# Optimization experiments

Measured on AMD Instinct MI355X. Metric: run time of the kernel, lower is better.

The kernel has to match this reference:

```python
import math
import jax, jax.numpy as jnp
import numpy as np

K = 4          # beats_per_bar
POS_DIM = 32   # fourier pos-embed dim


def setup_inputs() -> dict:
    key = jax.random.key(0)
    k1, k2, k3 = jax.random.split(key, 3)
    B, M, D = 8, 8192, 1024
    beat_emb = jax.random.normal(k1, (B, M, D), dtype=jnp.float32)
    W = jax.random.normal(k2, (D, D + POS_DIM), dtype=jnp.float32) * 0.02  # nn.Linear weight [out, in]
    b = jax.random.normal(k3, (D,), dtype=jnp.float32) * 0.02
    return {"beat_emb": beat_emb, "W": W, "b": b}


def _fourier_features(pos, dim):
    # pos: [Mb] in [0,1] -> [Mb, dim] (dim even, so no zero-pad branch needed)
    half = dim // 2
    freqs = jnp.exp(jnp.linspace(0.0, math.log(1000.0), half)).astype(pos.dtype)
    ang = pos[:, None] * freqs  # [Mb, half]
    return jnp.concatenate([jnp.sin(ang), jnp.cos(ang)], axis=-1)


def reference(beat_emb, W, b):
    B, M, D = beat_emb.shape
    Mb = (M + K - 1) // K
    pad = Mb * K - M
    x = jnp.pad(beat_emb, ((0, 0), (0, pad), (0, 0))) if pad else beat_emb
    # fused segment mean: [B, Mb, K, D] -> sum -> divide by actual segment length
    sums = x.reshape(B, Mb, K, D).sum(axis=2)
    counts = jnp.minimum(K, M - jnp.arange(Mb) * K).astype(beat_emb.dtype)  # [Mb]
    out = sums / counts[None, :, None]  # [B, Mb, D]
    # fourier positional features on normalized bar index (same for every batch row)
    idx = jnp.arange(Mb, dtype=beat_emb.dtype)
    pos = jnp.clip(idx / max(1, Mb - 1), 0.0, 1.0)
    ff = _fourier_features(pos, POS_DIM)                     # [Mb, POS_DIM]
    ff = jnp.broadcast_to(ff[None], (B, Mb, POS_DIM))
    h = jnp.concatenate([out, ff], axis=-1)                  # [B, Mb, D+POS_DIM]
    return jnp.einsum('bmi,oi->bmo', h, W) + b               # Linear: x @ W.T + b
```

## Files before the change

kernel.cpp:

```cpp
#include <hip/hip_runtime.h>
#include <math.h>
#include <stdint.h>
#include <stddef.h>

typedef short bf16x8 __attribute__((ext_vector_type(8)));
typedef short bf16x4 __attribute__((ext_vector_type(4)));
typedef float f32x4  __attribute__((ext_vector_type(4)));

#define BATCH   8
#define D_IN    1024
#define POSD    32
#define KD      1056
#define KP      1088
#define MBARS   2048
#define MROWS   16384
#define NOUT    1024

__device__ __forceinline__ short f2bf(float f) {
    unsigned u = __builtin_bit_cast(unsigned, f);
    u += 0x7fffu + ((u >> 16) & 1u);
    return (short)(u >> 16);
}

__device__ __forceinline__ void async_load16(const short* g, short* l) {
    __builtin_amdgcn_global_load_lds((__attribute__((address_space(1))) void*)g,
                                     (__attribute__((address_space(3))) void*)l,
                                     16, 0, 0);
}

__global__ __launch_bounds__(256) void prep(const float* __restrict__ x,
                                            const float* __restrict__ W,
                                            short* __restrict__ h,
                                            short* __restrict__ Wb) {
    const int t = threadIdx.x;
    const int bid = blockIdx.x;
    if (bid < MROWS) {
        const float4* src = (const float4*)(x + (size_t)bid * 4096);
        float4 s0 = src[t], s1 = src[t + 256], s2 = src[t + 512], s3 = src[t + 768];
        bf16x4 o = { f2bf((s0.x + s1.x + s2.x + s3.x) * 0.25f),
                     f2bf((s0.y + s1.y + s2.y + s3.y) * 0.25f),
                     f2bf((s0.z + s1.z + s2.z + s3.z) * 0.25f),
                     f2bf((s0.w + s1.w + s2.w + s3.w) * 0.25f) };
        short* hr = h + (size_t)bid * KP;
        *(bf16x4*)(hr + t * 4) = o;
        if (t < POSD) {
            const int mb = bid & (MBARS - 1);
            float pos = (float)mb * (1.0f / (float)(MBARS - 1));
            float fr  = expf((float)(t & 15) * (6.907755278982137f / 15.0f));
            float ang = pos * fr;
            hr[D_IN + t] = f2bf((t < 16) ? sinf(ang) : cosf(ang));
            hr[KD + t]   = 0;
        }
    } else {
        const int r = bid - MROWS;
        const float* wr = W + (size_t)r * KD;
        short* br = Wb + (size_t)r * KP;
        float4 v = *(const float4*)(wr + t * 4);
        bf16x4 o = { f2bf(v.x), f2bf(v.y), f2bf(v.z), f2bf(v.w) };
        *(bf16x4*)(br + t * 4) = o;
        if (t < 8) {
            float4 u = *(const float4*)(wr + 1024 + t * 4);
            bf16x4 p = { f2bf(u.x), f2bf(u.y), f2bf(u.z), f2bf(u.w) };
            *(bf16x4*)(br + 1024 + t * 4) = p;
            *(bf16x4*)(br + KD + t * 4)   = (bf16x4){0, 0, 0, 0};
        }
    }
}

__global__ __launch_bounds__(256) void gemm_bt(const short* __restrict__ A,
                                               const short* __restrict__ B,
                                               const float* __restrict__ bias,
                                               float* __restrict__ C) {
    __shared__ short As[128 * 64];
    __shared__ short Bs[128 * 64];

    const int tid  = threadIdx.x;
    const int wave = tid >> 6;
    const int lane = tid & 63;
    const int wrow = wave >> 1;
    const int wcol = wave & 1;

    const int m0 = blockIdx.x * 128;
    const int n0 = blockIdx.y * 128;

    const int r8   = tid >> 3;
    const int soct = (tid & 7) ^ (r8 & 7);
    const short* ag = A + (size_t)(m0 + r8) * KP + soct * 8;
    const short* bg = B + (size_t)(n0 + r8) * KP + soct * 8;
    short* al = As + wave * 512;
    short* bl = Bs + wave * 512;

    const int r  = lane & 15;
    const int q  = lane >> 4;
    const int rx = r & 7;
    const short* afr = As + (wrow * 64 + r) * 64;
    const short* bfr = Bs + (wcol * 64 + r) * 64;
    const int sl0 = ((q    ) ^ rx) * 8;
    const int sl1 = ((4 + q) ^ rx) * 8;

    f32x4 acc[4][4] = {};

    for (int k0 = 0; k0 < KP; k0 += 64) {
        __syncthreads();
#pragma unroll
        for (int i = 0; i < 4; ++i) {
            async_load16(ag + k0 + (size_t)i * 32 * KP, al + i * 2048);
            async_load16(bg + k0 + (size_t)i * 32 * KP, bl + i * 2048);
        }
        __syncthreads();

#pragma unroll
        for (int s = 0; s < 2; ++s) {
            const int sl = s ? sl1 : sl0;
            bf16x8 a[4], b[4];
#pragma unroll
            for (int i = 0; i < 4; ++i) {
                a[i] = *(const bf16x8*)(afr + i * 1024 + sl);
                b[i] = *(const bf16x8*)(bfr + i * 1024 + sl);
            }
#pragma unroll
            for (int i = 0; i < 4; ++i)
#pragma unroll
                for (int j = 0; j < 4; ++j)
                    acc[i][j] = __builtin_amdgcn_mfma_f32_16x16x32_bf16(a[i], b[j], acc[i][j], 0, 0, 0);
        }
    }

    const int rr0 = m0 + wrow * 64 + (q << 2);
    const int c0  = n0 + wcol * 64 + r;
    float bv[4];
#pragma unroll
    for (int j = 0; j < 4; ++j) bv[j] = bias[c0 + j * 16];
#pragma unroll
    for (int i = 0; i < 4; ++i)
#pragma unroll
        for (int rg = 0; rg < 4; ++rg) {
            float* cp = C + (size_t)(rr0 + i * 16 + rg) * NOUT;
#pragma unroll
            for (int j = 0; j < 4; ++j)
                cp[c0 + j * 16] = acc[i][j][rg] + bv[j];
        }
}

extern "C" void kernel_launch(void* const* d_in, const int* in_sizes, int n_in,
                              void* d_out, int out_size, void* d_ws, size_t ws_size,
                              hipStream_t stream) {
    const float* x    = (const float*)d_in[0];
    const float* W    = (const float*)d_in[1];
    const float* bias = (const float*)d_in[2];
    float* out = (float*)d_out;

    short* Wb = (short*)d_ws;
    short* h  = (short*)((char*)d_ws + (size_t)NOUT * KP * sizeof(short));

    prep   <<<dim3(MROWS + NOUT), dim3(256), 0, stream>>>(x, W, h, Wb);
    gemm_bt<<<dim3(MROWS / 128, NOUT / 128), dim3(256), 0, stream>>>(h, Wb, bias, out);
}
```

Measured before the change: 423.0 us.

## Fuse segment-mean into GEMM and precompute Fourier-feature projection table

The segment-mean reduction and bf16 conversion move into the GEMM's A-tile load, so the intermediate h matrix is no longer written to and re-read from global memory. The Fourier-feature columns are removed from the GEMM's K dimension. Their contribution is precomputed once per bar as a 2048x1024 fp32 table with the bias folded in, then added in the epilogue. The GEMM now uses 64-row by full-1024-column tiles with 512 threads, holding the whole W slice in LDS. In exchange, occupancy is low, W traffic per block is large, and the x loads are synchronous with no double buffering.

Result: slower. 466.3 us (+10.2%).

```diff
diff --git a/kernel.cpp b/kernel.cpp
--- a/kernel.cpp
+++ b/kernel.cpp
@@ -8,10 +8,9 @@
 typedef float f32x4  __attribute__((ext_vector_type(4)));
 
 #define BATCH   8
-#define D_IN    1024
+#define D       1024
 #define POSD    32
-#define KD      1056
-#define KP      1088
+#define WIN     1056
 #define MBARS   2048
 #define MROWS   16384
 #define NOUT    1024
@@ -28,117 +27,134 @@
                                      16, 0, 0);
 }
 
-__global__ __launch_bounds__(256) void prep(const float* __restrict__ x,
-                                            const float* __restrict__ W,
-                                            short* __restrict__ h,
-                                            short* __restrict__ Wb) {
-    const int t = threadIdx.x;
+__global__ __launch_bounds__(256) void prep2(const float* __restrict__ W,
+                                             const float* __restrict__ bias,
+                                             short* __restrict__ Wb,
+                                             float* __restrict__ FFW) {
+    const int t   = threadIdx.x;
     const int bid = blockIdx.x;
-    if (bid < MROWS) {
-        const float4* src = (const float4*)(x + (size_t)bid * 4096);
-        float4 s0 = src[t], s1 = src[t + 256], s2 = src[t + 512], s3 = src[t + 768];
-        bf16x4 o = { f2bf((s0.x + s1.x + s2.x + s3.x) * 0.25f),
-                     f2bf((s0.y + s1.y + s2.y + s3.y) * 0.25f),
-                     f2bf((s0.z + s1.z + s2.z + s3.z) * 0.25f),
-                     f2bf((s0.w + s1.w + s2.w + s3.w) * 0.25f) };
-        short* hr = h + (size_t)bid * KP;
-        *(bf16x4*)(hr + t * 4) = o;
-        if (t < POSD) {
-            const int mb = bid & (MBARS - 1);
-            float pos = (float)mb * (1.0f / (float)(MBARS - 1));
-            float fr  = expf((float)(t & 15) * (6.907755278982137f / 15.0f));
-            float ang = pos * fr;
-            hr[D_IN + t] = f2bf((t < 16) ? sinf(ang) : cosf(ang));
-            hr[KD + t]   = 0;
+    if (bid < NOUT) {
+        const float* wr = W + (size_t)bid * WIN;
+        float4 v = ((const float4*)wr)[t];
+        bf16x4 o = { f2bf(v.x), f2bf(v.y), f2bf(v.z), f2bf(v.w) };
+        *(bf16x4*)(Wb + (size_t)bid * D + t * 4) = o;
+    } else {
+        const int mb0 = (bid - NOUT) * 8;
+        __shared__ float ff[8][32];
+        if (t < 32) {
+            float fr = expf((float)(t & 15) * (6.907755278982137f / 15.0f));
+#pragma unroll
+            for (int e = 0; e < 8; ++e) {
+                float pos = (float)(mb0 + e) * (1.0f / (float)(MBARS - 1));
+                float ang = pos * fr;
+                ff[e][t] = (t < 16) ? sinf(ang) : cosf(ang);
+            }
         }
-    } else {
-        const int r = bid - MROWS;
-        const float* wr = W + (size_t)r * KD;
-        short* br = Wb + (size_t)r * KP;
-        float4 v = *(const float4*)(wr + t * 4);
-        bf16x4 o = { f2bf(v.x), f2bf(v.y), f2bf(v.z), f2bf(v.w) };
-        *(bf16x4*)(br + t * 4) = o;
-        if (t < 8) {
-            float4 u = *(const float4*)(wr + 1024 + t * 4);
-            bf16x4 p = { f2bf(u.x), f2bf(u.y), f2bf(u.z), f2bf(u.w) };
-            *(bf16x4*)(br + 1024 + t * 4) = p;
-            *(bf16x4*)(br + KD + t * 4)   = (bf16x4){0, 0, 0, 0};
+        __syncthreads();
+#pragma unroll
+        for (int u = 0; u < 4; ++u) {
+            const int n = t + u * 256;
+            const float* wp = W + (size_t)n * WIN + D;
+            float4 wv[8];
+#pragma unroll
+            for (int blk = 0; blk < 8; ++blk) wv[blk] = ((const float4*)wp)[blk];
+            const float bn = bias[n];
+#pragma unroll
+            for (int e = 0; e < 8; ++e) {
+                float s = bn;
+#pragma unroll
+                for (int blk = 0; blk < 8; ++blk) {
+                    s += ff[e][blk * 4 + 0] * wv[blk].x + ff[e][blk * 4 + 1] * wv[blk].y
+                       + ff[e][blk * 4 + 2] * wv[blk].z + ff[e][blk * 4 + 3] * wv[blk].w;
+                }
+                FFW[(size_t)(mb0 + e) * NOUT + n] = s;
+            }
         }
     }
 }
 
-__global__ __launch_bounds__(256) void gemm_bt(const short* __restrict__ A,
-                                               const short* __restrict__ B,
-                                               const float* __restrict__ bias,
-                                               float* __restrict__ C) {
-    __shared__ short As[128 * 64];
-    __shared__ short Bs[128 * 64];
+__global__ __launch_bounds__(512, 2) void fused(const float* __restrict__ x,
+                                                const short* __restrict__ Wb,
+                                                const float* __restrict__ FFW,
+                                                float* __restrict__ out) {
+    __shared__ short As[64 * 64];
+    __shared__ short Bs[1024 * 64];
 
     const int tid  = threadIdx.x;
     const int wave = tid >> 6;
     const int lane = tid & 63;
-    const int wrow = wave >> 1;
-    const int wcol = wave & 1;
+    const int m0   = blockIdx.x * 64;
 
-    const int m0 = blockIdx.x * 128;
-    const int n0 = blockIdx.y * 128;
-
-    const int r8   = tid >> 3;
-    const int soct = (tid & 7) ^ (r8 & 7);
-    const short* ag = A + (size_t)(m0 + r8) * KP + soct * 8;
-    const short* bg = B + (size_t)(n0 + r8) * KP + soct * 8;
-    short* al = As + wave * 512;
+    const int ra = tid >> 3;
+    const int oa = tid & 7;
+    const float* xg = x + (size_t)(m0 + ra) * 4096 + oa * 8;
+    short* aw = As + ra * 64 + ((oa ^ (ra & 7)) << 3);
+    const short* bg = Wb + (size_t)ra * D + ((oa ^ (ra & 7)) << 3);
     short* bl = Bs + wave * 512;
 
     const int r  = lane & 15;
     const int q  = lane >> 4;
     const int rx = r & 7;
-    const short* afr = As + (wrow * 64 + r) * 64;
-    const short* bfr = Bs + (wcol * 64 + r) * 64;
-    const int sl0 = ((q    ) ^ rx) * 8;
-    const int sl1 = ((4 + q) ^ rx) * 8;
+    const short* afr = As + r * 64;
+    const short* bfr = Bs + (wave * 128 + r) * 64;
+    const int sl0 = ((q    ) ^ rx) << 3;
+    const int sl1 = ((4 + q) ^ rx) << 3;
 
-    f32x4 acc[4][4] = {};
+    f32x4 acc[4][8] = {};
 
-    for (int k0 = 0; k0 < KP; k0 += 64) {
+    for (int k0 = 0; k0 < D; k0 += 64) {
         __syncthreads();
+        float4 t00 = *(const float4*)(xg + k0);
+        float4 t01 = *(const float4*)(xg + k0 + 4);
+        float4 t10 = *(const float4*)(xg + k0 + 1024);
+        float4 t11 = *(const float4*)(xg + k0 + 1028);
+        float4 t20 = *(const float4*)(xg + k0 + 2048);
+        float4 t21 = *(const float4*)(xg + k0 + 2052);
+        float4 t30 = *(const float4*)(xg + k0 + 3072);
+        float4 t31 = *(const float4*)(xg + k0 + 3076);
 #pragma unroll
-        for (int i = 0; i < 4; ++i) {
-            async_load16(ag + k0 + (size_t)i * 32 * KP, al + i * 2048);
-            async_load16(bg + k0 + (size_t)i * 32 * KP, bl + i * 2048);
-        }
+        for (int i = 0; i < 16; ++i)
+            async_load16(bg + k0 + (size_t)i * 64 * D, bl + i * 4096);
+        bf16x8 av = { f2bf((t00.x + t10.x + t20.x + t30.x) * 0.25f),
+                      f2bf((t00.y + t10.y + t20.y + t30.y) * 0.25f),
+                      f2bf((t00.z + t10.z + t20.z + t30.z) * 0.25f),
+                      f2bf((t00.w + t10.w + t20.w + t30.w) * 0.25f),
+                      f2bf((t01.x + t11.x + t21.x + t31.x) * 0.25f),
+                      f2bf((t01.y + t11.y + t21.y + t31.y) * 0.25f),
+                      f2bf((t01.z + t11.z + t21.z + t31.z) * 0.25f),
+                      f2bf((t01.w + t11.w + t21.w + t31.w) * 0.25f) };
+        *(bf16x8*)aw = av;
         __syncthreads();
 
 #pragma unroll
         for (int s = 0; s < 2; ++s) {
             const int sl = s ? sl1 : sl0;
-            bf16x8 a[4], b[4];
+            bf16x8 a[4], b[8];
 #pragma unroll
-            for (int i = 0; i < 4; ++i) {
-                a[i] = *(const bf16x8*)(afr + i * 1024 + sl);
-                b[i] = *(const bf16x8*)(bfr + i * 1024 + sl);
-            }
+            for (int i = 0; i < 4; ++i) a[i] = *(const bf16x8*)(afr + i * 1024 + sl);
+#pragma unroll
+            for (int j = 0; j < 8; ++j) b[j] = *(const bf16x8*)(bfr + j * 1024 + sl);
 #pragma unroll
             for (int i = 0; i < 4; ++i)
 #pragma unroll
-                for (int j = 0; j < 4; ++j)
+                for (int j = 0; j < 8; ++j)
                     acc[i][j] = __builtin_amdgcn_mfma_f32_16x16x32_bf16(a[i], b[j], acc[i][j], 0, 0, 0);
         }
     }
 
-    const int rr0 = m0 + wrow * 64 + (q << 2);
-    const int c0  = n0 + wcol * 64 + r;
-    float bv[4];
-#pragma unroll
-    for (int j = 0; j < 4; ++j) bv[j] = bias[c0 + j * 16];
+    const int mbb = m0 & (MBARS - 1);
+    const int c0  = wave * 128 + r;
+    const int rt0 = q << 2;
 #pragma unroll
     for (int i = 0; i < 4; ++i)
 #pragma unroll
         for (int rg = 0; rg < 4; ++rg) {
-            float* cp = C + (size_t)(rr0 + i * 16 + rg) * NOUT;
+            const int rt = i * 16 + rt0 + rg;
+            const float* fw = FFW + (size_t)(mbb + rt) * NOUT + c0;
+            float* cp = out + (size_t)(m0 + rt) * NOUT + c0;
 #pragma unroll
-            for (int j = 0; j < 4; ++j)
-                cp[c0 + j * 16] = acc[i][j][rg] + bv[j];
+            for (int j = 0; j < 8; ++j)
+                cp[j * 16] = acc[i][j][rg] + fw[j * 16];
         }
 }
 
@@ -150,9 +166,9 @@
     const float* bias = (const float*)d_in[2];
     float* out = (float*)d_out;
 
-    short* Wb = (short*)d_ws;
-    short* h  = (short*)((char*)d_ws + (size_t)NOUT * KP * sizeof(short));
+    short* Wb  = (short*)d_ws;
+    float* FFW = (float*)((char*)d_ws + (size_t)NOUT * D * sizeof(short));
 
-    prep   <<<dim3(MROWS + NOUT), dim3(256), 0, stream>>>(x, W, h, Wb);
-    gemm_bt<<<dim3(MROWS / 128, NOUT / 128), dim3(256), 0, stream>>>(h, Wb, bias, out);
+    prep2<<<dim3(NOUT + MBARS / 8), dim3(256), 0, stream>>>(W, bias, Wb, FFW);
+    fused<<<dim3(MROWS / 64), dim3(512), 0, stream>>>(x, Wb, FFW, out);
 }
```

## Precompute Fourier-feature projection plus bias per bar, shrink GEMM K to 1024

Applied to the files above, without the earlier changes.

Since the positional Fourier features are identical for every batch row, their product with the last 32 columns of W plus the bias is precomputed once per bar into an [MBARS, NOUT] float table. The main bf16 GEMM then runs over K=1024 instead of the padded 1088, which removes one of the 17 K-tiles. The epilogue adds the table entry for each row instead of the bias. The cost is an 8 MB fp32 table read in the epilogue and an extra small matmul in the prep kernel.

Measured after the change: 434.5 us. +2.7%, slower.

```diff
diff --git a/kernel.cpp b/kernel.cpp
--- a/kernel.cpp
+++ b/kernel.cpp
@@ -8,10 +8,9 @@
 typedef float f32x4  __attribute__((ext_vector_type(4)));
 
 #define BATCH   8
-#define D_IN    1024
+#define D       1024
 #define POSD    32
-#define KD      1056
-#define KP      1088
+#define WIN     1056
 #define MBARS   2048
 #define MROWS   16384
 #define NOUT    1024
@@ -28,11 +27,13 @@
                                      16, 0, 0);
 }
 
-__global__ __launch_bounds__(256) void prep(const float* __restrict__ x,
-                                            const float* __restrict__ W,
-                                            short* __restrict__ h,
-                                            short* __restrict__ Wb) {
-    const int t = threadIdx.x;
+__global__ __launch_bounds__(256) void prep3(const float* __restrict__ x,
+                                             const float* __restrict__ W,
+                                             const float* __restrict__ bias,
+                                             short* __restrict__ h,
+                                             short* __restrict__ Wb,
+                                             float* __restrict__ FFW) {
+    const int t   = threadIdx.x;
     const int bid = blockIdx.x;
     if (bid < MROWS) {
         const float4* src = (const float4*)(x + (size_t)bid * 4096);
@@ -41,35 +42,50 @@
                      f2bf((s0.y + s1.y + s2.y + s3.y) * 0.25f),
                      f2bf((s0.z + s1.z + s2.z + s3.z) * 0.25f),
                      f2bf((s0.w + s1.w + s2.w + s3.w) * 0.25f) };
-        short* hr = h + (size_t)bid * KP;
-        *(bf16x4*)(hr + t * 4) = o;
-        if (t < POSD) {
-            const int mb = bid & (MBARS - 1);
-            float pos = (float)mb * (1.0f / (float)(MBARS - 1));
-            float fr  = expf((float)(t & 15) * (6.907755278982137f / 15.0f));
-            float ang = pos * fr;
-            hr[D_IN + t] = f2bf((t < 16) ? sinf(ang) : cosf(ang));
-            hr[KD + t]   = 0;
+        *(bf16x4*)(h + (size_t)bid * D + t * 4) = o;
+    } else if (bid < MROWS + NOUT) {
+        const int rw = bid - MROWS;
+        float4 v = ((const float4*)(W + (size_t)rw * WIN))[t];
+        bf16x4 o = { f2bf(v.x), f2bf(v.y), f2bf(v.z), f2bf(v.w) };
+        *(bf16x4*)(Wb + (size_t)rw * D + t * 4) = o;
+    } else {
+        const int mb0 = (bid - MROWS - NOUT) * 8;
+        __shared__ float ff[8][32];
+        if (t < 32) {
+            float fr = expf((float)(t & 15) * (6.907755278982137f / 15.0f));
+#pragma unroll
+            for (int e = 0; e < 8; ++e) {
+                float pos = (float)(mb0 + e) * (1.0f / (float)(MBARS - 1));
+                float ang = pos * fr;
+                ff[e][t] = (t < 16) ? sinf(ang) : cosf(ang);
+            }
         }
-    } else {
-        const int r = bid - MROWS;
-        const float* wr = W + (size_t)r * KD;
-        short* br = Wb + (size_t)r * KP;
-        float4 v = *(const float4*)(wr + t * 4);
-        bf16x4 o = { f2bf(v.x), f2bf(v.y), f2bf(v.z), f2bf(v.w) };
-        *(bf16x4*)(br + t * 4) = o;
-        if (t < 8) {
-            float4 u = *(const float4*)(wr + 1024 + t * 4);
-            bf16x4 p = { f2bf(u.x), f2bf(u.y), f2bf(u.z), f2bf(u.w) };
-            *(bf16x4*)(br + 1024 + t * 4) = p;
-            *(bf16x4*)(br + KD + t * 4)   = (bf16x4){0, 0, 0, 0};
+        __syncthreads();
+#pragma unroll
+        for (int u = 0; u < 4; ++u) {
+            const int n = t + u * 256;
+            const float* wp = W + (size_t)n * WIN + D;
+            float4 wv[8];
+#pragma unroll
+            for (int blk = 0; blk < 8; ++blk) wv[blk] = ((const float4*)wp)[blk];
+            const float bn = bias[n];
+#pragma unroll
+            for (int e = 0; e < 8; ++e) {
+                float s = bn;
+#pragma unroll
+                for (int blk = 0; blk < 8; ++blk) {
+                    s += ff[e][blk * 4 + 0] * wv[blk].x + ff[e][blk * 4 + 1] * wv[blk].y
+                       + ff[e][blk * 4 + 2] * wv[blk].z + ff[e][blk * 4 + 3] * wv[blk].w;
+                }
+                FFW[(size_t)(mb0 + e) * NOUT + n] = s;
+            }
         }
     }
 }
 
 __global__ __launch_bounds__(256) void gemm_bt(const short* __restrict__ A,
                                                const short* __restrict__ B,
-                                               const float* __restrict__ bias,
+                                               const float* __restrict__ FFW,
                                                float* __restrict__ C) {
     __shared__ short As[128 * 64];
     __shared__ short Bs[128 * 64];
@@ -85,8 +101,8 @@
 
     const int r8   = tid >> 3;
     const int soct = (tid & 7) ^ (r8 & 7);
-    const short* ag = A + (size_t)(m0 + r8) * KP + soct * 8;
-    const short* bg = B + (size_t)(n0 + r8) * KP + soct * 8;
+    const short* ag = A + (size_t)(m0 + r8) * D + soct * 8;
+    const short* bg = B + (size_t)(n0 + r8) * D + soct * 8;
     short* al = As + wave * 512;
     short* bl = Bs + wave * 512;
 
@@ -100,12 +116,12 @@
 
     f32x4 acc[4][4] = {};
 
-    for (int k0 = 0; k0 < KP; k0 += 64) {
+    for (int k0 = 0; k0 < D; k0 += 64) {
         __syncthreads();
 #pragma unroll
         for (int i = 0; i < 4; ++i) {
-            async_load16(ag + k0 + (size_t)i * 32 * KP, al + i * 2048);
-            async_load16(bg + k0 + (size_t)i * 32 * KP, bl + i * 2048);
+            async_load16(ag + k0 + (size_t)i * 32 * D, al + i * 2048);
+            async_load16(bg + k0 + (size_t)i * 32 * D, bl + i * 2048);
         }
         __syncthreads();
 
@@ -128,17 +144,16 @@
 
     const int rr0 = m0 + wrow * 64 + (q << 2);
     const int c0  = n0 + wcol * 64 + r;
-    float bv[4];
-#pragma unroll
-    for (int j = 0; j < 4; ++j) bv[j] = bias[c0 + j * 16];
 #pragma unroll
     for (int i = 0; i < 4; ++i)
 #pragma unroll
         for (int rg = 0; rg < 4; ++rg) {
-            float* cp = C + (size_t)(rr0 + i * 16 + rg) * NOUT;
+            const int row = rr0 + i * 16 + rg;
+            const float* fw = FFW + (size_t)(row & (MBARS - 1)) * NOUT + c0;
+            float* cp = C + (size_t)row * NOUT + c0;
 #pragma unroll
             for (int j = 0; j < 4; ++j)
-                cp[c0 + j * 16] = acc[i][j][rg] + bv[j];
+                cp[j * 16] = acc[i][j][rg] + fw[j * 16];
         }
 }
 
@@ -150,9 +165,10 @@
     const float* bias = (const float*)d_in[2];
     float* out = (float*)d_out;
 
-    short* Wb = (short*)d_ws;
-    short* h  = (short*)((char*)d_ws + (size_t)NOUT * KP * sizeof(short));
+    short* Wb  = (short*)d_ws;
+    float* FFW = (float*)((char*)d_ws + (size_t)NOUT * D * sizeof(short));
+    short* h   = (short*)((char*)FFW + (size_t)MBARS * NOUT * sizeof(float));
 
-    prep   <<<dim3(MROWS + NOUT), dim3(256), 0, stream>>>(x, W, h, Wb);
-    gemm_bt<<<dim3(MROWS / 128, NOUT / 128), dim3(256), 0, stream>>>(h, Wb, bias, out);
+    prep3  <<<dim3(MROWS + NOUT + MBARS / 8), dim3(256), 0, stream>>>(x, W, bias, h, Wb, FFW);
+    gemm_bt<<<dim3(MROWS / 128, NOUT / 128), dim3(256), 0, stream>>>(h, Wb, FFW, out);
 }
```
